# Kernel optimization log

Measured on AMD Instinct MI355X. Metric: run time of the kernel, lower is better.

Reference implementation:

```python
import jax, jax.numpy as jnp
import numpy as np

N = 576        # variable nodes (from filename wman_N0576)
MROWS = 144    # check nodes = N*(1 - 3/4)
ROW_DEG = 15   # check-node degree (WiMAX rate-3/4 style)
BATCH = 256
ITERS = 3


def _make_H():
    # deterministic binary parity-check matrix with fixed row degree >= 2
    rng = np.random.default_rng(0)
    cols = np.argsort(rng.random((MROWS, N)), axis=1)[:, :ROW_DEG]
    H = np.zeros((MROWS, N), dtype=np.float32)
    H[np.arange(MROWS)[:, None], cols] = 1.0
    return jnp.asarray(H)


def setup_inputs() -> dict:
    key = jax.random.key(0)
    r = jax.random.normal(key, (BATCH, N), dtype=jnp.float32)  # channel LLRs
    alpha = jnp.full((ITERS,), 0.7, dtype=jnp.float32)
    beta = jnp.full((ITERS,), 0.05, dtype=jnp.float32)
    return {"r": r, "H": _make_H(), "alpha": alpha, "beta": beta}


def _c_to_v(M, H, node_idx, alpha, beta):
    # min-sum check-to-variable messages with offset beta and scale alpha
    abs_M = jnp.abs(M)                                   # [B, MROWS, N]
    masked = jnp.where(H == 1.0, abs_M, jnp.inf)
    neg_top, idx = jax.lax.top_k(-masked, 2)             # two smallest per row
    min1 = -neg_top[..., 0:1]
    min2 = -neg_top[..., 1:2]
    idx1 = idx[..., 0:1]
    E_abs = jnp.where(node_idx == idx1, min2, min1)      # exclude-self min
    valid = jnp.where(H == 1.0, jnp.sign(M), 1.0)
    row_prod = jnp.prod(valid, axis=2, keepdims=True)    # total sign per check
    E_sign = row_prod * valid                            # exclude-self sign
    E = alpha * E_sign * jnp.maximum(0.0, E_abs - beta)
    return E * H


def reference(r, H, alpha, beta):
    node_idx = jnp.arange(N)[None, None, :]              # [1,1,N]
    M = H[None, :, :] * r[:, None, :]                    # initial v->c messages
    E = jnp.zeros_like(M)
    for it in range(ITERS):
        E = _c_to_v(M, H, node_idx, alpha[it], beta[it])
        sum_E = jnp.sum(E, axis=1, keepdims=True)        # [B,1,N]
        M = (r[:, None, :] + sum_E - E) * H[None, :, :]
    return r + jnp.sum(E, axis=1)                        # posterior LLRs [B,N]
```

## Files before the change

kernel.cpp:

```cpp
#include <hip/hip_runtime.h>

#define NVAR   576
#define NROW   144
#define DEG    15
#define NEDGE  (NROW * DEG)
#define NBATCH 256
#define NITER  3
#define NT     192
#define NWORD  9

__global__ void build_bits_kernel(const float* __restrict__ H,
                                  unsigned long long* __restrict__ bits) {
    int gid  = blockIdx.x * blockDim.x + threadIdx.x;
    int wid  = gid >> 6;
    int lane = gid & 63;
    if (wid >= NROW * NWORD) return;
    float h = H[wid * 64 + lane];
    unsigned long long m = __ballot(h != 0.0f);
    if (lane == 0) bits[wid] = m;
}

__launch_bounds__(NT, 1)
__global__ void ldpc_minsum_kernel(const float* __restrict__ r,
                                   const unsigned long long* __restrict__ bits,
                                   const float* __restrict__ alpha,
                                   const float* __restrict__ beta,
                                   float* __restrict__ out) {
    __shared__ float rs[NVAR];
    __shared__ float sA[NVAR];
    __shared__ float sB[NVAR];
    __shared__ short colsh[NROW * 16];

    const int b = blockIdx.x;
    const int t = threadIdx.x;

    float alr[NITER], ber[NITER];
    #pragma unroll
    for (int i = 0; i < NITER; ++i) { alr[i] = alpha[i]; ber[i] = beta[i]; }

    #pragma unroll
    for (int k = 0; k < 3; ++k) {
        int n = t + k * NT;
        rs[n] = r[b * NVAR + n];
        sA[n] = 0.0f;
    }

    if (t < NROW) {
        unsigned long long w[NWORD];
        #pragma unroll
        for (int i = 0; i < NWORD; ++i) w[i] = bits[t * NWORD + i];
        int k = 0;
        #pragma unroll
        for (int i = 0; i < NWORD; ++i) {
            unsigned long long bw = w[i];
            while (bw) {
                int p = __ffsll((long long)bw) - 1;
                bw &= bw - 1;
                colsh[t * 16 + k] = (short)(i * 64 + p);
                ++k;
            }
        }
    }
    __syncthreads();

    int   ci[DEG];
    float Mv[DEG], Ev[DEG], rc[DEG];
    if (t < NROW) {
        #pragma unroll
        for (int j = 0; j < DEG; ++j) ci[j] = (int)colsh[t * 16 + j];
        #pragma unroll
        for (int j = 0; j < DEG; ++j) { rc[j] = rs[ci[j]]; Mv[j] = rc[j]; }
    }

    #pragma unroll
    for (int it = 0; it < NITER; ++it) {
        float* sum = (it & 1) ? sB : sA;
        float* nxt = (it & 1) ? sA : sB;

        if (t < NROW) {
            float m1 = INFINITY, m2 = INFINITY, sg = 1.0f;
            int j1 = 0;
            #pragma unroll
            for (int j = 0; j < DEG; ++j) {
                float v = Mv[j];
                float a = fabsf(v);
                float s = (v > 0.0f) ? 1.0f : ((v < 0.0f) ? -1.0f : 0.0f);
                sg *= s;
                if (a < m1) { m2 = m1; m1 = a; j1 = j; }
                else if (a < m2) { m2 = a; }
            }
            #pragma unroll
            for (int j = 0; j < DEG; ++j) {
                float v = Mv[j];
                float s = (v > 0.0f) ? 1.0f : ((v < 0.0f) ? -1.0f : 0.0f);
                float eabs = (j == j1) ? m2 : m1;
                float e = alr[it] * sg * s * fmaxf(0.0f, eabs - ber[it]);
                Ev[j] = e;
                atomicAdd(&sum[ci[j]], e);
            }
        }
        __syncthreads();

        if (it == NITER - 1) {
            #pragma unroll
            for (int k = 0; k < 3; ++k) {
                int n = t + k * NT;
                out[b * NVAR + n] = rs[n] + sum[n];
            }
        } else {
            #pragma unroll
            for (int k = 0; k < 3; ++k) nxt[t + k * NT] = 0.0f;
            if (t < NROW) {
                #pragma unroll
                for (int j = 0; j < DEG; ++j)
                    Mv[j] = rc[j] + sum[ci[j]] - Ev[j];
            }
            __syncthreads();
        }
    }
}

extern "C" void kernel_launch(void* const* d_in, const int* in_sizes, int n_in,
                              void* d_out, int out_size, void* d_ws, size_t ws_size,
                              hipStream_t stream) {
    const float* r     = (const float*)d_in[0];
    const float* H     = (const float*)d_in[1];
    const float* alpha = (const float*)d_in[2];
    const float* beta  = (const float*)d_in[3];
    float* out = (float*)d_out;
    unsigned long long* bits = (unsigned long long*)d_ws;

    build_bits_kernel<<<(NROW * NWORD * 64 + 255) / 256, 256, 0, stream>>>(H, bits);
    ldpc_minsum_kernel<<<NBATCH, NT, 0, stream>>>(r, bits, alpha, beta, out);
}
```

Baseline: 76.50 us.

## Fuse H bitmask build into decoder kernel and split min search

Removes the separate bitmask-building kernel launch. Each decoder block now scans H directly with float4 loads and fills per-row column lists in shared memory using shared atomics, so column order within a row is no longer deterministic. To cope with that, the exclude-self minimum is identified by column index rather than slot position. The two-smallest search is also split into two independent chains that merge at the end, which shortens the serial dependency. The cost is that every block rereads the full H matrix (about 330 KB) from global memory or cache.

```diff
diff --git a/kernel.cpp b/kernel.cpp
--- a/kernel.cpp
+++ b/kernel.cpp
@@ -3,33 +3,23 @@
 #define NVAR   576
 #define NROW   144
 #define DEG    15
-#define NEDGE  (NROW * DEG)
 #define NBATCH 256
 #define NITER  3
 #define NT     192
-#define NWORD  9
-
-__global__ void build_bits_kernel(const float* __restrict__ H,
-                                  unsigned long long* __restrict__ bits) {
-    int gid  = blockIdx.x * blockDim.x + threadIdx.x;
-    int wid  = gid >> 6;
-    int lane = gid & 63;
-    if (wid >= NROW * NWORD) return;
-    float h = H[wid * 64 + lane];
-    unsigned long long m = __ballot(h != 0.0f);
-    if (lane == 0) bits[wid] = m;
-}
+#define NF4    (NVAR / 4)
+#define GSTEPS ((NROW * NF4) / (NT * 3))
 
 __launch_bounds__(NT, 1)
-__global__ void ldpc_minsum_kernel(const float* __restrict__ r,
-                                   const unsigned long long* __restrict__ bits,
-                                   const float* __restrict__ alpha,
-                                   const float* __restrict__ beta,
-                                   float* __restrict__ out) {
+__global__ void ldpc_fused_kernel(const float* __restrict__ r,
+                                  const float4* __restrict__ H4,
+                                  const float* __restrict__ alpha,
+                                  const float* __restrict__ beta,
+                                  float* __restrict__ out) {
     __shared__ float rs[NVAR];
     __shared__ float sA[NVAR];
     __shared__ float sB[NVAR];
     __shared__ short colsh[NROW * 16];
+    __shared__ int   cnt[NROW];
 
     const int b = blockIdx.x;
     const int t = threadIdx.x;
@@ -38,29 +28,36 @@
     #pragma unroll
     for (int i = 0; i < NITER; ++i) { alr[i] = alpha[i]; ber[i] = beta[i]; }
 
+    if (t < NROW) cnt[t] = 0;
     #pragma unroll
-    for (int k = 0; k < 3; ++k) {
-        int n = t + k * NT;
-        rs[n] = r[b * NVAR + n];
-        sA[n] = 0.0f;
+    for (int k = 0; k < 3; ++k) sA[t + k * NT] = 0.0f;
+    __syncthreads();
+
+    float rv[3];
+    #pragma unroll
+    for (int k = 0; k < 3; ++k) rv[k] = r[b * NVAR + t + k * NT];
+
+    int rj[3], cj[3];
+    #pragma unroll
+    for (int j = 0; j < 3; ++j) {
+        int x = t + j * NT;
+        rj[j] = x / NF4;
+        cj[j] = (x - rj[j] * NF4) * 4;
     }
-
-    if (t < NROW) {
-        unsigned long long w[NWORD];
+    for (int g = 0; g < GSTEPS; ++g) {
         #pragma unroll
-        for (int i = 0; i < NWORD; ++i) w[i] = bits[t * NWORD + i];
-        int k = 0;
-        #pragma unroll
-        for (int i = 0; i < NWORD; ++i) {
-            unsigned long long bw = w[i];
-            while (bw) {
-                int p = __ffsll((long long)bw) - 1;
-                bw &= bw - 1;
-                colsh[t * 16 + k] = (short)(i * 64 + p);
-                ++k;
-            }
+        for (int j = 0; j < 3; ++j) {
+            float4 v = H4[g * (NT * 3) + j * NT + t];
+            int row = (g << 2) + rj[j];
+            int cb  = cj[j];
+            if (v.x != 0.0f) colsh[row * 16 + atomicAdd(&cnt[row], 1)] = (short)cb;
+            if (v.y != 0.0f) colsh[row * 16 + atomicAdd(&cnt[row], 1)] = (short)(cb + 1);
+            if (v.z != 0.0f) colsh[row * 16 + atomicAdd(&cnt[row], 1)] = (short)(cb + 2);
+            if (v.w != 0.0f) colsh[row * 16 + atomicAdd(&cnt[row], 1)] = (short)(cb + 3);
         }
     }
+    #pragma unroll
+    for (int k = 0; k < 3; ++k) rs[t + k * NT] = rv[k];
     __syncthreads();
 
     int   ci[DEG];
@@ -78,23 +75,37 @@
         float* nxt = (it & 1) ? sA : sB;
 
         if (t < NROW) {
-            float m1 = INFINITY, m2 = INFINITY, sg = 1.0f;
-            int j1 = 0;
+            float m1a = INFINITY, m2a = INFINITY, m1b = INFINITY, m2b = INFINITY;
+            int   c1a = -1,       c1b = -1;
+            float sg = 1.0f;
             #pragma unroll
-            for (int j = 0; j < DEG; ++j) {
+            for (int j = 0; j < 8; ++j) {
                 float v = Mv[j];
                 float a = fabsf(v);
-                float s = (v > 0.0f) ? 1.0f : ((v < 0.0f) ? -1.0f : 0.0f);
-                sg *= s;
-                if (a < m1) { m2 = m1; m1 = a; j1 = j; }
-                else if (a < m2) { m2 = a; }
+                sg *= (v > 0.0f) ? 1.0f : ((v < 0.0f) ? -1.0f : 0.0f);
+                if (a < m1a) { m2a = m1a; m1a = a; c1a = ci[j]; }
+                else if (a < m2a) m2a = a;
             }
+            #pragma unroll
+            for (int j = 8; j < DEG; ++j) {
+                float v = Mv[j];
+                float a = fabsf(v);
+                sg *= (v > 0.0f) ? 1.0f : ((v < 0.0f) ? -1.0f : 0.0f);
+                if (a < m1b) { m2b = m1b; m1b = a; c1b = ci[j]; }
+                else if (a < m2b) m2b = a;
+            }
+            float m1, m2; int c1;
+            if (m1b < m1a) { m1 = m1b; c1 = c1b; m2 = fminf(m1a, m2b); }
+            else           { m1 = m1a; c1 = c1a; m2 = fminf(m1b, m2a); }
+
+            float asg = alr[it] * sg;
+            float th  = ber[it];
             #pragma unroll
             for (int j = 0; j < DEG; ++j) {
                 float v = Mv[j];
                 float s = (v > 0.0f) ? 1.0f : ((v < 0.0f) ? -1.0f : 0.0f);
-                float eabs = (j == j1) ? m2 : m1;
-                float e = alr[it] * sg * s * fmaxf(0.0f, eabs - ber[it]);
+                float eabs = (ci[j] == c1) ? m2 : m1;
+                float e = asg * s * fmaxf(0.0f, eabs - th);
                 Ev[j] = e;
                 atomicAdd(&sum[ci[j]], e);
             }
@@ -123,13 +134,11 @@
 extern "C" void kernel_launch(void* const* d_in, const int* in_sizes, int n_in,
                               void* d_out, int out_size, void* d_ws, size_t ws_size,
                               hipStream_t stream) {
-    const float* r     = (const float*)d_in[0];
-    const float* H     = (const float*)d_in[1];
-    const float* alpha = (const float*)d_in[2];
-    const float* beta  = (const float*)d_in[3];
+    const float* r      = (const float*)d_in[0];
+    const float4* H4    = (const float4*)d_in[1];
+    const float* alpha  = (const float*)d_in[2];
+    const float* beta   = (const float*)d_in[3];
     float* out = (float*)d_out;
-    unsigned long long* bits = (unsigned long long*)d_ws;
 
-    build_bits_kernel<<<(NROW * NWORD * 64 + 255) / 256, 256, 0, stream>>>(H, bits);
-    ldpc_minsum_kernel<<<NBATCH, NT, 0, stream>>>(r, bits, alpha, beta, out);
+    ldpc_fused_kernel<<<NBATCH, NT, 0, stream>>>(r, H4, alpha, beta, out);
 }
```

After: 118.3 us. 54.7% more time.

## Fuse H bit-packing into decoder and split each check row across four lanes

Applied to the files above, without the earlier changes.

Removes the separate bit-packing kernel launch. Each block now ballots the dense H matrix into shared memory itself, so every block rereads H (about 330 KB) from cache or memory. The block grows to 576 threads, and each check row is handled by four lanes holding up to four edges each. Per-row min1/min2/sign are combined with xor shuffles, and the excluded minimum is picked by comparing column indices. The goal is to cut launch overhead and the serial 15-edge loop per thread, at the cost of redundant H reads in every block.

```diff
diff --git a/kernel.cpp b/kernel.cpp
--- a/kernel.cpp
+++ b/kernel.cpp
@@ -3,56 +3,54 @@
 #define NVAR   576
 #define NROW   144
 #define DEG    15
-#define NEDGE  (NROW * DEG)
 #define NBATCH 256
 #define NITER  3
-#define NT     192
+#define NT     576
 #define NWORD  9
-
-__global__ void build_bits_kernel(const float* __restrict__ H,
-                                  unsigned long long* __restrict__ bits) {
-    int gid  = blockIdx.x * blockDim.x + threadIdx.x;
-    int wid  = gid >> 6;
-    int lane = gid & 63;
-    if (wid >= NROW * NWORD) return;
-    float h = H[wid * 64 + lane];
-    unsigned long long m = __ballot(h != 0.0f);
-    if (lane == 0) bits[wid] = m;
-}
+#define NWTOT  (NROW * NWORD)
+#define NWAVE  (NT / 64)
+#define WPW    (NWTOT / NWAVE)
 
 __launch_bounds__(NT, 1)
-__global__ void ldpc_minsum_kernel(const float* __restrict__ r,
-                                   const unsigned long long* __restrict__ bits,
-                                   const float* __restrict__ alpha,
-                                   const float* __restrict__ beta,
-                                   float* __restrict__ out) {
+__global__ void ldpc_kernel(const float* __restrict__ r,
+                            const float* __restrict__ H,
+                            const float* __restrict__ alpha,
+                            const float* __restrict__ beta,
+                            float* __restrict__ out) {
     __shared__ float rs[NVAR];
     __shared__ float sA[NVAR];
     __shared__ float sB[NVAR];
+    __shared__ unsigned long long bitsh[NWTOT];
     __shared__ short colsh[NROW * 16];
 
-    const int b = blockIdx.x;
-    const int t = threadIdx.x;
+    const int b    = blockIdx.x;
+    const int t    = threadIdx.x;
+    const int wave = t >> 6;
+    const int lane = t & 63;
 
     float alr[NITER], ber[NITER];
     #pragma unroll
     for (int i = 0; i < NITER; ++i) { alr[i] = alpha[i]; ber[i] = beta[i]; }
 
-    #pragma unroll
-    for (int k = 0; k < 3; ++k) {
-        int n = t + k * NT;
-        rs[n] = r[b * NVAR + n];
-        sA[n] = 0.0f;
+    rs[t] = r[b * NVAR + t];
+    sA[t] = 0.0f;
+
+    {
+        const float* Hw = H + (wave * WPW) * 64 + lane;
+        #pragma unroll 4
+        for (int s = 0; s < WPW; ++s) {
+            float h = Hw[s * 64];
+            unsigned long long m = __ballot(h != 0.0f);
+            if (lane == 0) bitsh[wave * WPW + s] = m;
+        }
     }
+    __syncthreads();
 
     if (t < NROW) {
-        unsigned long long w[NWORD];
-        #pragma unroll
-        for (int i = 0; i < NWORD; ++i) w[i] = bits[t * NWORD + i];
         int k = 0;
         #pragma unroll
         for (int i = 0; i < NWORD; ++i) {
-            unsigned long long bw = w[i];
+            unsigned long long bw = bitsh[t * NWORD + i];
             while (bw) {
                 int p = __ffsll((long long)bw) - 1;
                 bw &= bw - 1;
@@ -63,13 +61,19 @@
     }
     __syncthreads();
 
-    int   ci[DEG];
-    float Mv[DEG], Ev[DEG], rc[DEG];
-    if (t < NROW) {
-        #pragma unroll
-        for (int j = 0; j < DEG; ++j) ci[j] = (int)colsh[t * 16 + j];
-        #pragma unroll
-        for (int j = 0; j < DEG; ++j) { rc[j] = rs[ci[j]]; Mv[j] = rc[j]; }
+    const int rr = t >> 2;
+    const int e  = t & 3;
+    const int ne = (e == 3) ? 3 : 4;
+
+    int   ci[4];
+    float Mv[4], Ev[4], rc[4];
+    #pragma unroll
+    for (int jj = 0; jj < 4; ++jj)
+        ci[jj] = (jj < ne) ? (int)colsh[rr * 16 + (e * 4 + jj)] : 0;
+    #pragma unroll
+    for (int jj = 0; jj < 4; ++jj) {
+        rc[jj] = rs[ci[jj]];
+        Mv[jj] = (jj < ne) ? rc[jj] : INFINITY;
     }
 
     #pragma unroll
@@ -77,44 +81,47 @@
         float* sum = (it & 1) ? sB : sA;
         float* nxt = (it & 1) ? sA : sB;
 
-        if (t < NROW) {
-            float m1 = INFINITY, m2 = INFINITY, sg = 1.0f;
-            int j1 = 0;
-            #pragma unroll
-            for (int j = 0; j < DEG; ++j) {
-                float v = Mv[j];
-                float a = fabsf(v);
-                float s = (v > 0.0f) ? 1.0f : ((v < 0.0f) ? -1.0f : 0.0f);
-                sg *= s;
-                if (a < m1) { m2 = m1; m1 = a; j1 = j; }
-                else if (a < m2) { m2 = a; }
-            }
-            #pragma unroll
-            for (int j = 0; j < DEG; ++j) {
-                float v = Mv[j];
-                float s = (v > 0.0f) ? 1.0f : ((v < 0.0f) ? -1.0f : 0.0f);
-                float eabs = (j == j1) ? m2 : m1;
-                float e = alr[it] * sg * s * fmaxf(0.0f, eabs - ber[it]);
-                Ev[j] = e;
-                atomicAdd(&sum[ci[j]], e);
-            }
+        float m1 = INFINITY, m2 = INFINITY, sg = 1.0f;
+        int   c1 = -1;
+        #pragma unroll
+        for (int jj = 0; jj < 4; ++jj) {
+            float v = Mv[jj];
+            float a = fabsf(v);
+            sg *= (v > 0.0f) ? 1.0f : ((v < 0.0f) ? -1.0f : 0.0f);
+            if (a < m1) { m2 = m1; m1 = a; c1 = ci[jj]; }
+            else if (a < m2) m2 = a;
+        }
+        #pragma unroll
+        for (int d = 1; d <= 2; d <<= 1) {
+            float om1 = __shfl_xor(m1, d);
+            float om2 = __shfl_xor(m2, d);
+            int   oc1 = __shfl_xor(c1, d);
+            float osg = __shfl_xor(sg, d);
+            sg *= osg;
+            if (om1 < m1) { m2 = fminf(m1, om2); m1 = om1; c1 = oc1; }
+            else          { m2 = fminf(m2, om1); }
+        }
+
+        float asg = alr[it] * sg;
+        float th  = ber[it];
+        #pragma unroll
+        for (int jj = 0; jj < 4; ++jj) {
+            float v = Mv[jj];
+            float s = (v > 0.0f) ? 1.0f : ((v < 0.0f) ? -1.0f : 0.0f);
+            float eabs = (ci[jj] == c1) ? m2 : m1;
+            float ev = asg * s * fmaxf(0.0f, eabs - th);
+            Ev[jj] = ev;
+            if (jj < ne) atomicAdd(&sum[ci[jj]], ev);
         }
         __syncthreads();
 
         if (it == NITER - 1) {
+            out[b * NVAR + t] = rs[t] + sum[t];
+        } else {
+            nxt[t] = 0.0f;
             #pragma unroll
-            for (int k = 0; k < 3; ++k) {
-                int n = t + k * NT;
-                out[b * NVAR + n] = rs[n] + sum[n];
-            }
-        } else {
-            #pragma unroll
-            for (int k = 0; k < 3; ++k) nxt[t + k * NT] = 0.0f;
-            if (t < NROW) {
-                #pragma unroll
-                for (int j = 0; j < DEG; ++j)
-                    Mv[j] = rc[j] + sum[ci[j]] - Ev[j];
-            }
+            for (int jj = 0; jj < 4; ++jj)
+                if (jj < ne) Mv[jj] = rc[jj] + sum[ci[jj]] - Ev[jj];
             __syncthreads();
         }
     }
@@ -128,8 +135,6 @@
     const float* alpha = (const float*)d_in[2];
     const float* beta  = (const float*)d_in[3];
     float* out = (float*)d_out;
-    unsigned long long* bits = (unsigned long long*)d_ws;
 
-    build_bits_kernel<<<(NROW * NWORD * 64 + 255) / 256, 256, 0, stream>>>(H, bits);
-    ldpc_minsum_kernel<<<NBATCH, NT, 0, stream>>>(r, bits, alpha, beta, out);
+    ldpc_kernel<<<NBATCH, NT, 0, stream>>>(r, H, alpha, beta, out);
 }
```

Measured after the change: 114.7 us. +49.9%, slower.
